# Optimization experiments

Hardware: AMD Instinct MI355X
Metric: run time of the kernel (lower is better)

The kernel has to match this reference:

```python
import jax, jax.numpy as jnp
import numpy as np

N, E, P = 20000, 640000, 200000
IN_DIM, HID, HEADS, OUT_DIM = 256, 64, 4, 86
NEG_SLOPE = 0.2


def _gat_layer(h_in, src, dst, W, a_src, a_dst, b, heads, concat):
    n = h_in.shape[0]
    c = W.shape[1] // heads
    h = (h_in @ W).reshape(n, heads, c)                      # [N,H,C]
    alpha_s = jnp.sum(h * a_src, axis=-1)                    # [N,H]
    alpha_d = jnp.sum(h * a_dst, axis=-1)                    # [N,H]
    e = alpha_s[src] + alpha_d[dst]                          # [E,H]
    e = jnp.where(e > 0, e, NEG_SLOPE * e)                   # leaky_relu(0.2)
    # softmax over incoming edges of each destination node
    m = jax.ops.segment_max(e, dst, num_segments=n)          # [N,H]
    e = jnp.exp(e - m[dst])
    denom = jax.ops.segment_sum(e, dst, num_segments=n)      # [N,H]
    w = e / denom[dst]                                       # [E,H]
    msg = h[src] * w[:, :, None]                             # [E,H,C]
    out = jax.ops.segment_sum(msg, dst, num_segments=n)      # [N,H,C]
    if concat:
        out = out.reshape(n, heads * c)
    else:
        out = out.mean(axis=1)
    return out + b


def setup_inputs() -> dict:
    key = jax.random.key(0)
    ks = jax.random.split(key, 16)
    s = lambda *d: 1.0 / np.sqrt(d[0])
    x = jax.random.normal(ks[0], (N, IN_DIM), jnp.float32)
    edge_index = jax.random.randint(ks[1], (2, E), 0, N, jnp.int32)
    drug_pairs = jax.random.randint(ks[2], (P, 2), 0, N, jnp.int32)
    W1 = jax.random.normal(ks[3], (IN_DIM, HEADS * HID), jnp.float32) * s(IN_DIM)
    a_src1 = jax.random.normal(ks[4], (HEADS, HID), jnp.float32) * s(HID)
    a_dst1 = jax.random.normal(ks[5], (HEADS, HID), jnp.float32) * s(HID)
    b1 = jnp.zeros((HEADS * HID,), jnp.float32)
    W2 = jax.random.normal(ks[6], (HEADS * HID, HID), jnp.float32) * s(HEADS * HID)
    a_src2 = jax.random.normal(ks[7], (1, HID), jnp.float32) * s(HID)
    a_dst2 = jax.random.normal(ks[8], (1, HID), jnp.float32) * s(HID)
    b2 = jnp.zeros((HID,), jnp.float32)
    Wp1 = jax.random.normal(ks[9], (2 * HID, HID), jnp.float32) * s(2 * HID)
    bp1 = jnp.zeros((HID,), jnp.float32)
    Wp2 = jax.random.normal(ks[10], (HID, OUT_DIM), jnp.float32) * s(HID)
    bp2 = jnp.zeros((OUT_DIM,), jnp.float32)
    return dict(x=x, edge_index=edge_index, drug_pairs=drug_pairs,
                W1=W1, a_src1=a_src1, a_dst1=a_dst1, b1=b1,
                W2=W2, a_src2=a_src2, a_dst2=a_dst2, b2=b2,
                Wp1=Wp1, bp1=bp1, Wp2=Wp2, bp2=bp2)


def reference(x, edge_index, drug_pairs, W1, a_src1, a_dst1, b1,
              W2, a_src2, a_dst2, b2, Wp1, bp1, Wp2, bp2):
    n = x.shape[0]
    # PyG GATConv default add_self_loops=True
    loop = jnp.arange(n, dtype=edge_index.dtype)
    src = jnp.concatenate([edge_index[0], loop])
    dst = jnp.concatenate([edge_index[1], loop])
    h = _gat_layer(x, src, dst, W1, a_src1, a_dst1, b1, HEADS, concat=True)
    h = jax.nn.elu(h)  # dropout is identity in eval mode
    h = _gat_layer(h, src, dst, W2, a_src2, a_dst2, b2, 1, concat=False)
    h = jax.nn.elu(h)
    combined = jnp.concatenate([h[drug_pairs[:, 0]], h[drug_pairs[:, 1]]], axis=1)
    z = jax.nn.relu(combined @ Wp1 + bp1)
    return z @ Wp2 + bp2
```

## Files before the change

### kernel.cpp

```cpp
#include <hip/hip_runtime.h>
#include <hip/hip_fp16.h>

#define NN 20000
#define NE 640000
#define NEE 660000
#define NP 200000
#define NEG 0.2f

typedef _Float16 f16;
typedef __attribute__((ext_vector_type(4))) _Float16 f16x4;
typedef __attribute__((ext_vector_type(8))) _Float16 f16x8;
typedef __attribute__((ext_vector_type(4))) float f32x4;

__global__ void k_hist(const int* __restrict__ ei, int* __restrict__ cnt) {
  int i = blockIdx.x * 256 + threadIdx.x;
  if (i >= NEE) return;
  int d = (i < NE) ? ei[NE + i] : (i - NE);
  atomicAdd(&cnt[d], 1);
}

__global__ __launch_bounds__(1024) void k_scan(const int* __restrict__ cnt, int* __restrict__ rp) {
  __shared__ int ps[1024];
  const int CH = 20;
  int t = threadIdx.x;
  int lo = t * CH, hi = lo + CH;
  if (hi > NN) hi = NN;
  if (lo > NN) lo = NN;
  int s = 0;
  for (int i = lo; i < hi; ++i) s += cnt[i];
  ps[t] = s;
  __syncthreads();
  for (int off = 1; off < 1024; off <<= 1) {
    int v = (t >= off) ? ps[t - off] : 0;
    __syncthreads();
    ps[t] += v;
    __syncthreads();
  }
  int run = (t > 0) ? ps[t - 1] : 0;
  for (int i = lo; i < hi; ++i) { rp[i] = run; run += cnt[i]; }
  if (t == 1023) rp[NN] = ps[1023];
}

__global__ void k_scatter(const int* __restrict__ ei, const int* __restrict__ rp,
                          int* __restrict__ cur, int* __restrict__ col,
                          int* __restrict__ dstv) {
  int i = blockIdx.x * 256 + threadIdx.x;
  if (i >= NEE) return;
  int s, d;
  if (i < NE) { s = ei[i]; d = ei[NE + i]; } else { s = i - NE; d = s; }
  int pos = atomicAdd(&cur[d], 1);
  col[rp[d] + pos] = s;
  dstv[rp[d] + pos] = d;
}

__global__ void k_prep(const float* __restrict__ Wp2, const float* __restrict__ bp2,
                       const float* __restrict__ W2, const float* __restrict__ W1,
                       f16* __restrict__ Wp2Th, float* __restrict__ bp2p,
                       f16* __restrict__ W2T, f16* __restrict__ W1T) {
  int i = blockIdx.x * 256 + threadIdx.x;
  if (i < 96 * 64) {
    int o = i >> 6, t = i & 63;
    Wp2Th[o * 64 + t] = (o < 86) ? (f16)Wp2[t * 86 + o] : (f16)0.f;
  }
  if (i < 96) bp2p[i] = (i < 86) ? bp2[i] : 0.f;
  if (i < 64 * 256) {
    int n = i >> 8, k = i & 255;
    W2T[n * 256 + k] = (f16)W2[k * 64 + n];
  }
  if (i < 256 * 256) {
    int r = i >> 8, c = i & 255;
    W1T[c * 256 + r] = (f16)W1[i];
  }
}

__global__ __launch_bounds__(256) void k_gemm1(
    const float* __restrict__ x, const f16* __restrict__ W1T,
    const float* __restrict__ as1, const float* __restrict__ ad1,
    __half* __restrict__ h1h16, float* __restrict__ AS1, float* __restrict__ AD1) {
  __shared__ f16 xs[16][264];
  int tid = threadIdx.x;
  int base = blockIdx.x * 16;
  {
    int r = tid >> 4, ch = tid & 15;
    const float4* src = (const float4*)(x + (size_t)(base + r) * 256 + ch * 16);
    float4 a0 = src[0], a1 = src[1], a2 = src[2], a3 = src[3];
    f16 tmp[16];
    tmp[0] = (f16)a0.x; tmp[1] = (f16)a0.y; tmp[2] = (f16)a0.z; tmp[3] = (f16)a0.w;
    tmp[4] = (f16)a1.x; tmp[5] = (f16)a1.y; tmp[6] = (f16)a1.z; tmp[7] = (f16)a1.w;
    tmp[8] = (f16)a2.x; tmp[9] = (f16)a2.y; tmp[10] = (f16)a2.z; tmp[11] = (f16)a2.w;
    tmp[12] = (f16)a3.x; tmp[13] = (f16)a3.y; tmp[14] = (f16)a3.z; tmp[15] = (f16)a3.w;
    *(uint4*)&xs[r][ch * 16] = *(uint4*)&tmp[0];
    *(uint4*)&xs[r][ch * 16 + 8] = *(uint4*)&tmp[8];
  }
  __syncthreads();
  int wv = tid >> 6, lane = tid & 63;
  int head = wv;
  int lr = lane & 15, lk = lane >> 4;
  f32x4 acc[4] = {{0.f,0.f,0.f,0.f},{0.f,0.f,0.f,0.f},{0.f,0.f,0.f,0.f},{0.f,0.f,0.f,0.f}};
#pragma unroll
  for (int k0 = 0; k0 < 256; k0 += 32) {
    f16x8 a = *(const f16x8*)&xs[lr][k0 + lk * 8];
#pragma unroll
    for (int nt = 0; nt < 4; ++nt) {
      int n = head * 64 + nt * 16 + lr;
      f16x8 b = *(const f16x8*)(W1T + (size_t)n * 256 + k0 + lk * 8);
      acc[nt] = __builtin_amdgcn_mfma_f32_16x16x32_f16(a, b, acc[nt], 0, 0, 0);
    }
  }
#pragma unroll
  for (int nt = 0; nt < 4; ++nt) {
    int cc = nt * 16 + lr;
#pragma unroll
    for (int r = 0; r < 4; ++r) {
      int row = lk * 4 + r;
      h1h16[((size_t)head * NN + base + row) * 64 + cc] = __float2half(acc[nt][r]);
    }
  }
#pragma unroll
  for (int r = 0; r < 4; ++r) {
    float ps = 0.f, pd = 0.f;
#pragma unroll
    for (int nt = 0; nt < 4; ++nt) {
      int cc = nt * 16 + lr;
      ps += acc[nt][r] * as1[head * 64 + cc];
      pd += acc[nt][r] * ad1[head * 64 + cc];
    }
#pragma unroll
    for (int off = 1; off < 16; off <<= 1) {
      ps += __shfl_xor(ps, off);
      pd += __shfl_xor(pd, off);
    }
    if (lr == 0) {
      int n = base + lk * 4 + r;
      AS1[n * 4 + head] = ps;
      AD1[n * 4 + head] = pd;
    }
  }
}

__global__ void k_edgew1(const int* __restrict__ col, const int* __restrict__ dstv,
                         const float* __restrict__ AS1, const float* __restrict__ AD1,
                         float* __restrict__ w1) {
  int i = blockIdx.x * 256 + threadIdx.x;
  if (i >= NEE) return;
  int s = col[i], d = dstv[i];
  float4 as = *(const float4*)(AS1 + s * 4);
  float4 ad = *(const float4*)(AD1 + d * 4);
  float e0 = as.x + ad.x, e1 = as.y + ad.y, e2 = as.z + ad.z, e3 = as.w + ad.w;
  e0 = fmaxf(e0, NEG * e0);
  e1 = fmaxf(e1, NEG * e1);
  e2 = fmaxf(e2, NEG * e2);
  e3 = fmaxf(e3, NEG * e3);
  w1[0 * NEE + i] = __expf(e0);
  w1[1 * NEE + i] = __expf(e1);
  w1[2 * NEE + i] = __expf(e2);
  w1[3 * NEE + i] = __expf(e3);
}

__global__ __launch_bounds__(256, 4) void k_agg1(
    const int* __restrict__ rp, const int* __restrict__ col,
    const float* __restrict__ w1, const __half* __restrict__ h1h16,
    const float* __restrict__ b1, __half* __restrict__ out16) {
  int b = blockIdx.x;
  int xcd = b & 7;
  int head = xcd >> 1;
  int grp = (b >> 3) * 2 + (xcd & 1);
  int wave = threadIdx.x >> 6, lane = threadIdx.x & 63;
  int n = grp * 4 + wave;
  int g = lane >> 3, c8 = (lane & 7) * 8;
  int e0 = rp[n], e1 = rp[n + 1];
  const __half* hs = h1h16 + (size_t)head * NN * 64;
  const float* wp = w1 + (size_t)head * NEE;
  float acc[8] = {0.f,0.f,0.f,0.f,0.f,0.f,0.f,0.f};
  float den = 0.f;

  int ee = e0 + g;
  bool v = ee < e1;
  int ec = v ? ee : e1 - 1;
  int s = col[ec];
  float pw = v ? wp[ec] : 0.f;

  for (int e = e0; e < e1; e += 8) {
    int een = e + 8 + g;
    bool vn = een < e1;
    int ecn = vn ? een : e1 - 1;
    int sn = col[ecn];
    float pwn = vn ? wp[ecn] : 0.f;
    float4 raw = *(const float4*)(hs + (size_t)s * 64 + c8);
    const f16* hf = (const f16*)&raw;
#pragma unroll
    for (int i = 0; i < 8; ++i) acc[i] += pw * (float)hf[i];
    den += pw;
    s = sn; pw = pwn;
  }
#pragma unroll
  for (int i = 0; i < 8; ++i) {
    acc[i] += __shfl_xor(acc[i], 8);
    acc[i] += __shfl_xor(acc[i], 16);
    acc[i] += __shfl_xor(acc[i], 32);
  }
  den += __shfl_xor(den, 8); den += __shfl_xor(den, 16); den += __shfl_xor(den, 32);
  if (lane < 8) {
    float inv = 1.f / den;
    int cbase = head * 64 + lane * 8;
    __half ho[8];
#pragma unroll
    for (int i = 0; i < 8; ++i) {
      float r = acc[i] * inv + b1[cbase + i];
      r = r > 0.f ? r : __expf(r) - 1.f;
      ho[i] = __float2half(r);
    }
    *(uint4*)(out16 + (size_t)n * 256 + cbase) = *(uint4*)&ho[0];
  }
}

__global__ __launch_bounds__(256) void k_gemm2(
    const f16* __restrict__ h1a16, const f16* __restrict__ W2T,
    const float* __restrict__ as2, const float* __restrict__ ad2,
    __half* __restrict__ h2h16, float* __restrict__ AS2, float* __restrict__ AD2) {
  __shared__ f16 xs[16][264];
  __shared__ float psL[4][16], pdL[4][16];
  int tid = threadIdx.x;
  int base = blockIdx.x * 16;
  {
    int r = tid >> 4, ch = tid & 15;
    const uint4* src = (const uint4*)(h1a16 + (size_t)(base + r) * 256 + ch * 16);
    uint4 v0 = src[0], v1 = src[1];
    *(uint4*)&xs[r][ch * 16] = v0;
    *(uint4*)&xs[r][ch * 16 + 8] = v1;
  }
  __syncthreads();
  int wv = tid >> 6, lane = tid & 63;
  int lr = lane & 15, lk = lane >> 4;
  f32x4 acc = {0.f, 0.f, 0.f, 0.f};
#pragma unroll
  for (int k0 = 0; k0 < 256; k0 += 32) {
    f16x8 a = *(const f16x8*)&xs[lr][k0 + lk * 8];
    f16x8 b = *(const f16x8*)(W2T + (size_t)(wv * 16 + lr) * 256 + k0 + lk * 8);
    acc = __builtin_amdgcn_mfma_f32_16x16x32_f16(a, b, acc, 0, 0, 0);
  }
  int cc = wv * 16 + lr;
  float asv = as2[cc], adv = ad2[cc];
  float psr[4], pdr[4];
#pragma unroll
  for (int r = 0; r < 4; ++r) {
    int row = lk * 4 + r;
    h2h16[(size_t)(base + row) * 64 + cc] = __float2half(acc[r]);
    float ps = acc[r] * asv, pd = acc[r] * adv;
#pragma unroll
    for (int off = 1; off < 16; off <<= 1) {
      ps += __shfl_xor(ps, off);
      pd += __shfl_xor(pd, off);
    }
    psr[r] = ps; pdr[r] = pd;
  }
  if (lr == 0) {
#pragma unroll
    for (int r = 0; r < 4; ++r) {
      psL[wv][lk * 4 + r] = psr[r];
      pdL[wv][lk * 4 + r] = pdr[r];
    }
  }
  __syncthreads();
  if (tid < 16) {
    AS2[base + tid] = psL[0][tid] + psL[1][tid] + psL[2][tid] + psL[3][tid];
    AD2[base + tid] = pdL[0][tid] + pdL[1][tid] + pdL[2][tid] + pdL[3][tid];
  }
}

__global__ void k_edgew2(const int* __restrict__ col, const int* __restrict__ dstv,
                         const float* __restrict__ AS2, const float* __restrict__ AD2,
                         float* __restrict__ w2) {
  int i = blockIdx.x * 256 + threadIdx.x;
  if (i >= NEE) return;
  int s = col[i], d = dstv[i];
  float ev = AS2[s] + AD2[d];
  ev = fmaxf(ev, NEG * ev);
  w2[i] = __expf(ev);
}

__global__ __launch_bounds__(256, 4) void k_agg2(
    const int* __restrict__ rp, const int* __restrict__ col,
    const float* __restrict__ w2, const __half* __restrict__ h2h16,
    const float* __restrict__ b2, float* __restrict__ out) {
  int wave = threadIdx.x >> 6, lane = threadIdx.x & 63;
  int n = blockIdx.x * 4 + wave;
  int g = lane >> 3, c8 = (lane & 7) * 8;
  int e0 = rp[n], e1 = rp[n + 1];
  float acc[8] = {0.f,0.f,0.f,0.f,0.f,0.f,0.f,0.f};
  float den = 0.f;

  int ee = e0 + g;
  bool v = ee < e1;
  int ec = v ? ee : e1 - 1;
  int s = col[ec];
  float pw = v ? w2[ec] : 0.f;

  for (int e = e0; e < e1; e += 8) {
    int een = e + 8 + g;
    bool vn = een < e1;
    int ecn = vn ? een : e1 - 1;
    int sn = col[ecn];
    float pwn = vn ? w2[ecn] : 0.f;
    float4 raw = *(const float4*)(h2h16 + (size_t)s * 64 + c8);
    const f16* hf = (const f16*)&raw;
#pragma unroll
    for (int i = 0; i < 8; ++i) acc[i] += pw * (float)hf[i];
    den += pw;
    s = sn; pw = pwn;
  }
#pragma unroll
  for (int i = 0; i < 8; ++i) {
    acc[i] += __shfl_xor(acc[i], 8);
    acc[i] += __shfl_xor(acc[i], 16);
    acc[i] += __shfl_xor(acc[i], 32);
  }
  den += __shfl_xor(den, 8); den += __shfl_xor(den, 16); den += __shfl_xor(den, 32);
  if (lane < 8) {
    float inv = 1.f / den;
    int cbase = lane * 8;
    float o[8];
#pragma unroll
    for (int i = 0; i < 8; ++i) {
      float r = acc[i] * inv + b2[cbase + i];
      o[i] = r > 0.f ? r : __expf(r) - 1.f;
    }
    *(float4*)(out + (size_t)n * 64 + cbase) = *(float4*)&o[0];
    *(float4*)(out + (size_t)n * 64 + cbase + 4) = *(float4*)&o[4];
  }
}

__global__ __launch_bounds__(128) void k_predot(
    const float* __restrict__ h2a, const float* __restrict__ Wp1,
    const float* __restrict__ bp1, float* __restrict__ AB) {
  __shared__ float xsT[64][20];
  int c = threadIdx.x;
  int base = blockIdx.x * 16;
  for (int i = threadIdx.x; i < 16 * 64; i += 128) {
    int r = i >> 6, k = i & 63;
    xsT[k][r] = h2a[(size_t)(base + r) * 64 + k];
  }
  __syncthreads();
  int part = c >> 6, u = c & 63;
  float bv = (part == 0) ? bp1[u] : 0.f;
  float acc[16];
#pragma unroll
  for (int r = 0; r < 16; ++r) acc[r] = bv;
#pragma unroll 2
  for (int k = 0; k < 64; ++k) {
    float wv = Wp1[(size_t)(part * 64 + k) * 64 + u];
    const float4* xr = (const float4*)&xsT[k][0];
    float4 x0 = xr[0], x1 = xr[1], x2 = xr[2], x3 = xr[3];
    acc[0] += x0.x * wv; acc[1] += x0.y * wv; acc[2] += x0.z * wv; acc[3] += x0.w * wv;
    acc[4] += x1.x * wv; acc[5] += x1.y * wv; acc[6] += x1.z * wv; acc[7] += x1.w * wv;
    acc[8] += x2.x * wv; acc[9] += x2.y * wv; acc[10] += x2.z * wv; acc[11] += x2.w * wv;
    acc[12] += x3.x * wv; acc[13] += x3.y * wv; acc[14] += x3.z * wv; acc[15] += x3.w * wv;
  }
#pragma unroll
  for (int r = 0; r < 16; ++r) AB[(size_t)(base + r) * 128 + c] = acc[r];
}

__global__ __launch_bounds__(256) void k_pairs(
    const int* __restrict__ pairs, const float* __restrict__ AB,
    const f16* __restrict__ Wp2Th, const float* __restrict__ bp2p,
    float* __restrict__ out) {
  __shared__ f16 zh[64][72];
  int tid = threadIdx.x;
  int pp = tid & 63, q = tid >> 6;
  int p = blockIdx.x * 64 + pp;
  int pi = pairs[2 * p], pj = pairs[2 * p + 1];

  {
    const float4* ar = (const float4*)(AB + (size_t)pi * 128 + q * 16);
    const float4* br = (const float4*)(AB + (size_t)pj * 128 + 64 + q * 16);
    f16 zv[16];
#pragma unroll
    for (int m = 0; m < 4; ++m) {
      float4 a = ar[m], b = br[m];
      zv[m * 4]     = (f16)fmaxf(a.x + b.x, 0.f);
      zv[m * 4 + 1] = (f16)fmaxf(a.y + b.y, 0.f);
      zv[m * 4 + 2] = (f16)fmaxf(a.z + b.z, 0.f);
      zv[m * 4 + 3] = (f16)fmaxf(a.w + b.w, 0.f);
    }
    *(uint4*)&zh[pp][q * 16] = *(uint4*)&zv[0];
    *(uint4*)&zh[pp][q * 16 + 8] = *(uint4*)&zv[8];
  }
  __syncthreads();

  int wv = tid >> 6, lane = tid & 63;
  int lr = lane & 15, lk = lane >> 4;
#pragma unroll
  for (int nt = 0; nt < 6; ++nt) {
    f32x4 acc = {0.f, 0.f, 0.f, 0.f};
#pragma unroll
    for (int k0 = 0; k0 < 64; k0 += 32) {
      f16x8 a = *(const f16x8*)&zh[wv * 16 + lr][k0 + lk * 8];
      f16x8 b = *(const f16x8*)(Wp2Th + (size_t)(nt * 16 + lr) * 64 + k0 + lk * 8);
      acc = __builtin_amdgcn_mfma_f32_16x16x32_f16(a, b, acc, 0, 0, 0);
    }
    int o = nt * 16 + lr;
    if (o < 86) {
      float bb = bp2p[o];
#pragma unroll
      for (int r = 0; r < 4; ++r) {
        int pr = blockIdx.x * 64 + wv * 16 + lk * 4 + r;
        out[(size_t)pr * 86 + o] = acc[r] + bb;
      }
    }
  }
}

extern "C" void kernel_launch(void* const* d_in, const int* in_sizes, int n_in,
                              void* d_out, int out_size, void* d_ws, size_t ws_size,
                              hipStream_t stream) {
  (void)in_sizes; (void)n_in; (void)out_size; (void)ws_size;
  const float* x      = (const float*)d_in[0];
  const int*   ei     = (const int*)d_in[1];
  const int*   pairs  = (const int*)d_in[2];
  const float* W1     = (const float*)d_in[3];
  const float* a_src1 = (const float*)d_in[4];
  const float* a_dst1 = (const float*)d_in[5];
  const float* b1     = (const float*)d_in[6];
  const float* W2     = (const float*)d_in[7];
  const float* a_src2 = (const float*)d_in[8];
  const float* a_dst2 = (const float*)d_in[9];
  const float* b2     = (const float*)d_in[10];
  const float* Wp1    = (const float*)d_in[11];
  const float* bp1    = (const float*)d_in[12];
  const float* Wp2    = (const float*)d_in[13];
  const float* bp2    = (const float*)d_in[14];
  float* out = (float*)d_out;

  char* w = (char*)d_ws;
  auto alloc = [&](size_t bytes) -> void* {
    void* pp = (void*)w;
    w += (bytes + 255) & ~(size_t)255;
    return pp;
  };
  __half* h1h16 = (__half*)alloc((size_t)NN * 256 * 2);
  float*  AS1   = (float*)alloc((size_t)NN * 4 * 4);
  float*  AD1   = (float*)alloc((size_t)NN * 4 * 4);
  __half* h1a16 = (__half*)alloc((size_t)NN * 256 * 2);
  __half* h2h16 = (__half*)alloc((size_t)NN * 64 * 2);
  float*  AS2   = (float*)alloc((size_t)NN * 4);
  float*  AD2   = (float*)alloc((size_t)NN * 4);
  float*  h2agg = (float*)alloc((size_t)NN * 64 * 4);
  float*  AB    = (float*)alloc((size_t)NN * 128 * 4);
  f16*    W1T   = (f16*)alloc((size_t)256 * 256 * 2);
  f16*    Wp2Th = (f16*)alloc((size_t)96 * 64 * 2);
  float*  bp2p  = (float*)alloc(96 * 4);
  f16*    W2T   = (f16*)alloc((size_t)64 * 256 * 2);
  float*  w1    = (float*)alloc((size_t)4 * NEE * 4);
  float*  w2    = (float*)alloc((size_t)NEE * 4);
  int*    rp    = (int*)alloc((size_t)(NN + 1) * 4);
  int*    cnt   = (int*)alloc((size_t)NN * 4);
  int*    cur   = (int*)alloc((size_t)NN * 4);
  int*    col   = (int*)alloc((size_t)NEE * 4);
  int*    dstv  = (int*)alloc((size_t)NEE * 4);

  (void)hipMemsetAsync(cnt, 0, (size_t)NN * 4, stream);
  (void)hipMemsetAsync(cur, 0, (size_t)NN * 4, stream);

  const int EB = (NEE + 255) / 256;
  k_hist<<<EB, 256, 0, stream>>>(ei, cnt);
  k_scan<<<1, 1024, 0, stream>>>(cnt, rp);
  k_scatter<<<EB, 256, 0, stream>>>(ei, rp, cur, col, dstv);
  k_prep<<<256, 256, 0, stream>>>(Wp2, bp2, W2, W1, Wp2Th, bp2p, W2T, W1T);

  k_gemm1<<<NN / 16, 256, 0, stream>>>(x, W1T, a_src1, a_dst1, h1h16, AS1, AD1);
  k_edgew1<<<EB, 256, 0, stream>>>(col, dstv, AS1, AD1, w1);
  k_agg1<<<NN, 256, 0, stream>>>(rp, col, w1, h1h16, b1, h1a16);

  k_gemm2<<<NN / 16, 256, 0, stream>>>((const f16*)h1a16, W2T, a_src2, a_dst2, h2h16, AS2, AD2);
  k_edgew2<<<EB, 256, 0, stream>>>(col, dstv, AS2, AD2, w2);
  k_agg2<<<NN / 4, 256, 0, stream>>>(rp, col, w2, h2h16, b2, h2agg);

  k_predot<<<NN / 16, 128, 0, stream>>>(h2agg, Wp1, bp1, AB);
  k_pairs<<<NP / 64, 256, 0, stream>>>(pairs, AB, Wp2Th, bp2p, out);
}
```

Measured before the change: 275.9 us.

## Partition CSR atomics by XCD node range and drop the per-edge dst array

The histogram and scatter kernels now launch 8 passes per edge chunk. Each pass only performs atomics for destination nodes in its own 2500-node range, which the blockIdx&7 mapping appears to place on one XCD so the atomics stay in a local L2 slice. The per-edge dst array is removed. The edge-weight kernels now walk CSR rows one wave per node and load the destination attention term once per node. The cost is re-reading the edge list eight times and lane underuse for low-degree nodes in the edge-weight kernels.

```diff
diff --git a/kernel.cpp b/kernel.cpp
--- a/kernel.cpp
+++ b/kernel.cpp
@@ -6,17 +6,28 @@
 #define NEE 660000
 #define NP 200000
 #define NEG 0.2f
+#define NPN 2500
 
 typedef _Float16 f16;
 typedef __attribute__((ext_vector_type(4))) _Float16 f16x4;
 typedef __attribute__((ext_vector_type(8))) _Float16 f16x8;
 typedef __attribute__((ext_vector_type(4))) float f32x4;
 
+#define ECHUNK 2048
+#define NCHUNK ((NEE + ECHUNK - 1) / ECHUNK)
+
 __global__ void k_hist(const int* __restrict__ ei, int* __restrict__ cnt) {
-  int i = blockIdx.x * 256 + threadIdx.x;
-  if (i >= NEE) return;
-  int d = (i < NE) ? ei[NE + i] : (i - NE);
-  atomicAdd(&cnt[d], 1);
+  int pass = blockIdx.x & 7;
+  int chunk = blockIdx.x >> 3;
+  int lo = pass * NPN, hi = lo + NPN;
+  int base = chunk * ECHUNK;
+#pragma unroll 1
+  for (int k = 0; k < ECHUNK; k += 256) {
+    int i = base + k + threadIdx.x;
+    if (i >= NEE) break;
+    int d = (i < NE) ? ei[NE + i] : (i - NE);
+    if (d >= lo && d < hi) atomicAdd(&cnt[d], 1);
+  }
 }
 
 __global__ __launch_bounds__(1024) void k_scan(const int* __restrict__ cnt, int* __restrict__ rp) {
@@ -42,15 +53,22 @@
 }
 
 __global__ void k_scatter(const int* __restrict__ ei, const int* __restrict__ rp,
-                          int* __restrict__ cur, int* __restrict__ col,
-                          int* __restrict__ dstv) {
-  int i = blockIdx.x * 256 + threadIdx.x;
-  if (i >= NEE) return;
-  int s, d;
-  if (i < NE) { s = ei[i]; d = ei[NE + i]; } else { s = i - NE; d = s; }
-  int pos = atomicAdd(&cur[d], 1);
-  col[rp[d] + pos] = s;
-  dstv[rp[d] + pos] = d;
+                          int* __restrict__ cur, int* __restrict__ col) {
+  int pass = blockIdx.x & 7;
+  int chunk = blockIdx.x >> 3;
+  int lo = pass * NPN, hi = lo + NPN;
+  int base = chunk * ECHUNK;
+#pragma unroll 1
+  for (int k = 0; k < ECHUNK; k += 256) {
+    int i = base + k + threadIdx.x;
+    if (i >= NEE) break;
+    int s, d;
+    if (i < NE) { s = ei[i]; d = ei[NE + i]; } else { s = i - NE; d = s; }
+    if (d >= lo && d < hi) {
+      int pos = atomicAdd(&cur[d], 1);
+      col[rp[d] + pos] = s;
+    }
+  }
 }
 
 __global__ void k_prep(const float* __restrict__ Wp2, const float* __restrict__ bp2,
@@ -138,23 +156,27 @@
   }
 }
 
-__global__ void k_edgew1(const int* __restrict__ col, const int* __restrict__ dstv,
-                         const float* __restrict__ AS1, const float* __restrict__ AD1,
-                         float* __restrict__ w1) {
-  int i = blockIdx.x * 256 + threadIdx.x;
-  if (i >= NEE) return;
-  int s = col[i], d = dstv[i];
-  float4 as = *(const float4*)(AS1 + s * 4);
-  float4 ad = *(const float4*)(AD1 + d * 4);
-  float e0 = as.x + ad.x, e1 = as.y + ad.y, e2 = as.z + ad.z, e3 = as.w + ad.w;
-  e0 = fmaxf(e0, NEG * e0);
-  e1 = fmaxf(e1, NEG * e1);
-  e2 = fmaxf(e2, NEG * e2);
-  e3 = fmaxf(e3, NEG * e3);
-  w1[0 * NEE + i] = __expf(e0);
-  w1[1 * NEE + i] = __expf(e1);
-  w1[2 * NEE + i] = __expf(e2);
-  w1[3 * NEE + i] = __expf(e3);
+__global__ __launch_bounds__(256) void k_edgew1(
+    const int* __restrict__ rp, const int* __restrict__ col,
+    const float* __restrict__ AS1, const float* __restrict__ AD1,
+    float* __restrict__ w1) {
+  int wave = threadIdx.x >> 6, lane = threadIdx.x & 63;
+  int n = blockIdx.x * 4 + wave;
+  int e0 = rp[n], e1 = rp[n + 1];
+  float4 ad = *(const float4*)(AD1 + n * 4);
+  for (int e = e0 + lane; e < e1; e += 64) {
+    int s = col[e];
+    float4 as = *(const float4*)(AS1 + s * 4);
+    float v0 = as.x + ad.x, v1 = as.y + ad.y, v2 = as.z + ad.z, v3 = as.w + ad.w;
+    v0 = fmaxf(v0, NEG * v0);
+    v1 = fmaxf(v1, NEG * v1);
+    v2 = fmaxf(v2, NEG * v2);
+    v3 = fmaxf(v3, NEG * v3);
+    w1[0 * NEE + e] = __expf(v0);
+    w1[1 * NEE + e] = __expf(v1);
+    w1[2 * NEE + e] = __expf(v2);
+    w1[3 * NEE + e] = __expf(v3);
+  }
 }
 
 __global__ __launch_bounds__(256, 4) void k_agg1(
@@ -268,15 +290,20 @@
   }
 }
 
-__global__ void k_edgew2(const int* __restrict__ col, const int* __restrict__ dstv,
-                         const float* __restrict__ AS2, const float* __restrict__ AD2,
-                         float* __restrict__ w2) {
-  int i = blockIdx.x * 256 + threadIdx.x;
-  if (i >= NEE) return;
-  int s = col[i], d = dstv[i];
-  float ev = AS2[s] + AD2[d];
-  ev = fmaxf(ev, NEG * ev);
-  w2[i] = __expf(ev);
+__global__ __launch_bounds__(256) void k_edgew2(
+    const int* __restrict__ rp, const int* __restrict__ col,
+    const float* __restrict__ AS2, const float* __restrict__ AD2,
+    float* __restrict__ w2) {
+  int wave = threadIdx.x >> 6, lane = threadIdx.x & 63;
+  int n = blockIdx.x * 4 + wave;
+  int e0 = rp[n], e1 = rp[n + 1];
+  float adv = AD2[n];
+  for (int e = e0 + lane; e < e1; e += 64) {
+    int s = col[e];
+    float ev = AS2[s] + adv;
+    ev = fmaxf(ev, NEG * ev);
+    w2[e] = __expf(ev);
+  }
 }
 
 __global__ __launch_bounds__(256, 4) void k_agg2(
@@ -456,23 +483,21 @@
   int*    cnt   = (int*)alloc((size_t)NN * 4);
   int*    cur   = (int*)alloc((size_t)NN * 4);
   int*    col   = (int*)alloc((size_t)NEE * 4);
-  int*    dstv  = (int*)alloc((size_t)NEE * 4);
 
   (void)hipMemsetAsync(cnt, 0, (size_t)NN * 4, stream);
   (void)hipMemsetAsync(cur, 0, (size_t)NN * 4, stream);
 
-  const int EB = (NEE + 255) / 256;
-  k_hist<<<EB, 256, 0, stream>>>(ei, cnt);
+  k_hist<<<NCHUNK * 8, 256, 0, stream>>>(ei, cnt);
   k_scan<<<1, 1024, 0, stream>>>(cnt, rp);
-  k_scatter<<<EB, 256, 0, stream>>>(ei, rp, cur, col, dstv);
+  k_scatter<<<NCHUNK * 8, 256, 0, stream>>>(ei, rp, cur, col);
   k_prep<<<256, 256, 0, stream>>>(Wp2, bp2, W2, W1, Wp2Th, bp2p, W2T, W1T);
 
   k_gemm1<<<NN / 16, 256, 0, stream>>>(x, W1T, a_src1, a_dst1, h1h16, AS1, AD1);
-  k_edgew1<<<EB, 256, 0, stream>>>(col, dstv, AS1, AD1, w1);
+  k_edgew1<<<NN / 4, 256, 0, stream>>>(rp, col, AS1, AD1, w1);
   k_agg1<<<NN, 256, 0, stream>>>(rp, col, w1, h1h16, b1, h1a16);
 
   k_gemm2<<<NN / 16, 256, 0, stream>>>((const f16*)h1a16, W2T, a_src2, a_dst2, h2h16, AS2, AD2);
-  k_edgew2<<<EB, 256, 0, stream>>>(col, dstv, AS2, AD2, w2);
+  k_edgew2<<<NN / 4, 256, 0, stream>>>(rp, col, AS2, AD2, w2);
   k_agg2<<<NN / 4, 256, 0, stream>>>(rp, col, w2, h2h16, b2, h2agg);
 
   k_predot<<<NN / 16, 128, 0, stream>>>(h2agg, Wp1, bp1, AB);
```

Result: no change. 273.2 us (-1.0%).
